# Kernel optimization log

Hardware: AMD Instinct MI355X
Metric: run time of the kernel (lower is better)

## Reference

```python
import jax, jax.numpy as jnp
import numpy as np
import math

BATCH, L, H, P = 8, 2048, 1024, 512
DT_MIN, DT_MAX = 1e-3, 1e-1
STEP_RESCALE = 1.0


def setup_inputs() -> dict:
    key = jax.random.key(0)
    ks = jax.random.split(key, 8)
    signal = jax.random.normal(ks[0], (BATCH, L, H), dtype=jnp.float32)
    prev_state = jnp.zeros((BATCH, P), dtype=jnp.float32)
    # S5-style init: Lambda_re < 0, Lambda_im = pi * k
    Lambda_re = -0.5 * jnp.ones((P,), dtype=jnp.float32)
    Lambda_im = math.pi * jnp.arange(P, dtype=jnp.float32)
    # B stored as real (P,H,2) -> complex B_tilde; lecun scale 1/sqrt(H)
    B = jax.random.normal(ks[1], (P, H, 2), dtype=jnp.float32) / math.sqrt(H)
    # C stored as real (H,P,2) -> complex C_tilde; lecun scale 1/sqrt(P)
    C = jax.random.normal(ks[2], (H, P, 2), dtype=jnp.float32) / math.sqrt(P)
    D = jax.random.normal(ks[3], (H,), dtype=jnp.float32)
    u = jax.random.uniform(ks[4], (P, 1), dtype=jnp.float32)
    log_step = u * (math.log(DT_MAX) - math.log(DT_MIN)) + math.log(DT_MIN)
    return {"signal": signal, "prev_state": prev_state,
            "Lambda_re": Lambda_re, "Lambda_im": Lambda_im,
            "B": B, "C": C, "D": D, "log_step": log_step}


def _binop(qi, qj):
    # parallel-scan combine for diagonal linear recurrence x_t = A_t x_{t-1} + b_t
    A_i, b_i = qi
    A_j, b_j = qj
    return (A_j * A_i, b_j + A_j * b_i)


def reference(signal, prev_state, Lambda_re, Lambda_im, B, C, D, log_step):
    Lambda = Lambda_re + 1j * Lambda_im                      # (P,) complex
    B_tilde = B[..., 0] + 1j * B[..., 1]                     # (P,H)
    C_tilde = C[..., 0] + 1j * C[..., 1]                     # (H,P)
    step = STEP_RESCALE * jnp.exp(log_step[:, 0])            # (P,)
    # zero-order hold discretization
    Lambda_bar = jnp.exp(Lambda * step)                      # (P,)
    B_bar = ((Lambda_bar - 1.0) / Lambda)[:, None] * B_tilde # (P,H)
    # Bu elements: (BATCH, L, P) complex
    Bu = jnp.einsum('blh,ph->blp', signal.astype(B_bar.dtype), B_bar)
    # A elements: Lambda_bar tiled over time; first element carries prev_state
    A_first = (Lambda_bar[None, :] * prev_state.astype(Lambda_bar.dtype))[:, None, :]
    A_rest = jnp.broadcast_to(Lambda_bar, (signal.shape[0], signal.shape[1] - 1, Lambda_bar.shape[0]))
    A = jnp.concatenate([A_first, A_rest], axis=1)           # (BATCH, L, P)
    _, xs = jax.lax.associative_scan(_binop, (A, Bu), axis=1)  # xs: (BATCH, L, P)
    # conj_sym=True -> 2 * Re(C_tilde @ x), plus feedthrough D*u
    y = 2.0 * jnp.einsum('blp,hp->blh', xs, C_tilde).real + D * signal
    state = xs[:, -1]                                        # (BATCH, P) complex
    return y, state
```

## Files before the change

kernel.cpp:

```cpp
#include <hip/hip_runtime.h>
#include <math.h>

#define L_SEQ   2048
#define BATCH_N 8
#define H_DIM   1024
#define P_DIM   512
#define M_DIM   (BATCH_N * L_SEQ)
#define N2      1024
#define NC      32
#define T_CHUNK 64

typedef __attribute__((ext_vector_type(8))) __bf16 bf16x8;
typedef __attribute__((ext_vector_type(4))) float f32x4;

__device__ __forceinline__ unsigned f2bf_bits(float f) {
    unsigned u = __builtin_bit_cast(unsigned, f);
    return (u + 0x7fffu + ((u >> 16) & 1u)) >> 16;
}
__device__ __forceinline__ float bf_lo(unsigned v) {
    return __builtin_bit_cast(float, v << 16);
}
__device__ __forceinline__ float bf_hi(unsigned v) {
    return __builtin_bit_cast(float, v & 0xffff0000u);
}
__device__ __forceinline__ float bf2f(unsigned short u) {
    return __builtin_bit_cast(float, (unsigned)u << 16);
}

#define ASYNC_COPY16(gsrc, ldst)                                            \
    __builtin_amdgcn_global_load_lds(                                       \
        (__attribute__((address_space(1))) void*)(gsrc),                    \
        (__attribute__((address_space(3))) void*)(ldst), 16, 0, 0)

__global__ void setup_lam(const float* __restrict__ Lre_in,
                          const float* __restrict__ Lim_in,
                          const float* __restrict__ log_step,
                          float* __restrict__ lam) {
    int p = blockIdx.x * blockDim.x + threadIdx.x;
    if (p >= P_DIM) return;
    float step = expf(log_step[p]);
    float c = Lre_in[p];
    float d = Lim_in[p];
    float mag = expf(c * step);
    float ang = d * step;
    float lr = mag * cosf(ang);
    float li = mag * sinf(ang);
    float a = lr - 1.0f, b = li;
    float inv = 1.0f / (c * c + d * d);
    lam[p]             = lr;
    lam[P_DIM + p]     = li;
    lam[2 * P_DIM + p] = (a * c + b * d) * inv;
    lam[3 * P_DIM + p] = (b * c - a * d) * inv;
}

__global__ void build_W(const float* __restrict__ B,
                        const float* __restrict__ C,
                        const float* __restrict__ lam,
                        unsigned short* __restrict__ W1,
                        unsigned short* __restrict__ W2) {
    int idx = blockIdx.x * blockDim.x + threadIdx.x;
    if (idx < P_DIM * H_DIM) {
        int p = idx >> 10;
        int h = idx & (H_DIM - 1);
        float bre = B[(size_t)idx * 2];
        float bim = B[(size_t)idx * 2 + 1];
        float gre = lam[2 * P_DIM + p];
        float gim = lam[3 * P_DIM + p];
        W1[(size_t)p * H_DIM + h]           = (unsigned short)f2bf_bits(gre * bre - gim * bim);
        W1[(size_t)(P_DIM + p) * H_DIM + h] = (unsigned short)f2bf_bits(gre * bim + gim * bre);
    } else {
        int j = idx - P_DIM * H_DIM;
        int h = j >> 9;
        int p = j & (P_DIM - 1);
        float cre = C[(size_t)j * 2];
        float cim = C[(size_t)j * 2 + 1];
        W2[(size_t)h * N2 + p]         = (unsigned short)f2bf_bits( 2.0f * cre);
        W2[(size_t)h * N2 + P_DIM + p] = (unsigned short)f2bf_bits(-2.0f * cim);
    }
}

__global__ void convert_sig(const float* __restrict__ in,
                            unsigned short* __restrict__ out) {
    size_t i = ((size_t)blockIdx.x * 256 + threadIdx.x) * 4;
    float4 v = *(const float4*)(in + i);
    ushort4 o;
    o.x = (unsigned short)f2bf_bits(v.x);
    o.y = (unsigned short)f2bf_bits(v.y);
    o.z = (unsigned short)f2bf_bits(v.z);
    o.w = (unsigned short)f2bf_bits(v.w);
    *(ushort4*)(out + i) = o;
}

template <int MODE>
__global__ __launch_bounds__(256, 4) void gemm_mfma(
    const unsigned short* __restrict__ A,
    const unsigned short* __restrict__ W,
    void* __restrict__ Out, int K,
    const float* __restrict__ Dvec, const unsigned short* __restrict__ SigBf)
{
    __shared__ unsigned short smem[128 * 64 * 2];
    unsigned short* As = smem;
    unsigned short* Ws = smem + 128 * 64;

    const int tid  = threadIdx.x;
    const int lane = tid & 63;
    const int wid  = tid >> 6;
    const int wm   = wid >> 1;
    const int wn   = wid & 1;

    const int id  = blockIdx.x;
    const int xcd = id & 7;
    const int j   = id >> 3;
    const int mb  = xcd * 16 + (j >> 3);
    const int nb  = j & 7;
    const int m0 = mb * 128;
    const int n0 = nb * 128;

    const int srow = tid >> 3;
    const int qg   = ((tid & 7) - ((tid >> 4) & 7)) & 7;
    const unsigned short* Abase = A + (size_t)(m0 + srow) * K + qg * 8;
    const unsigned short* Wbase = W + (size_t)(n0 + srow) * K + qg * 8;

    const int fr = lane & 15;
    const int fq = (lane >> 4) & 3;
    const int sw = fr >> 1;

    f32x4 acc[4][4] = {};

    for (int k0 = 0; k0 < K; k0 += 64) {
        __syncthreads();
        #pragma unroll
        for (int i = 0; i < 4; ++i)
            ASYNC_COPY16(Abase + (size_t)(i * 32) * K + k0,
                         As + (size_t)(i * 256 + wid * 64) * 8);
        #pragma unroll
        for (int i = 0; i < 4; ++i)
            ASYNC_COPY16(Wbase + (size_t)(i * 32) * K + k0,
                         Ws + (size_t)(i * 256 + wid * 64) * 8);
        __syncthreads();

        #pragma unroll
        for (int kk = 0; kk < 2; ++kk) {
            bf16x8 af[4], wf[4];
            #pragma unroll
            for (int mi = 0; mi < 4; ++mi) {
                int row = wm * 64 + mi * 16 + fr;
                int sl  = (kk * 4 + fq + sw) & 7;
                af[mi] = *(const bf16x8*)&As[(size_t)row * 64 + sl * 8];
            }
            #pragma unroll
            for (int ni = 0; ni < 4; ++ni) {
                int row = wn * 64 + ni * 16 + fr;
                int sl  = (kk * 4 + fq + sw) & 7;
                wf[ni] = *(const bf16x8*)&Ws[(size_t)row * 64 + sl * 8];
            }
            #pragma unroll
            for (int mi = 0; mi < 4; ++mi)
                #pragma unroll
                for (int ni = 0; ni < 4; ++ni)
                    acc[mi][ni] = __builtin_amdgcn_mfma_f32_16x16x32_bf16(
                        af[mi], wf[ni], acc[mi][ni], 0, 0, 0);
        }
    }

    if (MODE == 0) {
        unsigned short* T = smem;
        #pragma unroll
        for (int h = 0; h < 2; ++h) {
            __syncthreads();
            if (wm == h) {
                #pragma unroll
                for (int mi = 0; mi < 4; ++mi)
                    #pragma unroll
                    for (int ni = 0; ni < 4; ++ni)
                        #pragma unroll
                        for (int r = 0; r < 4; ++r) {
                            int lrow = mi * 16 + fq * 4 + r;
                            int lcol = wn * 64 + ni * 16 + fr;
                            T[lrow * 128 + lcol] =
                                (unsigned short)f2bf_bits(acc[mi][ni][r]);
                        }
            }
            __syncthreads();
            #pragma unroll
            for (int jj = 0; jj < 4; ++jj) {
                int chunk = jj * 256 + tid;
                int row = chunk >> 4;
                int co  = (chunk & 15) * 8;
                *(ulonglong2*)((unsigned short*)Out +
                    (size_t)(m0 + h * 64 + row) * 1024 + n0 + co) =
                    *(const ulonglong2*)&T[row * 128 + co];
            }
        }
    } else {
        float Dl[4];
        #pragma unroll
        for (int ni = 0; ni < 4; ++ni)
            Dl[ni] = Dvec[n0 + wn * 64 + ni * 16 + fr];
        #pragma unroll
        for (int mi = 0; mi < 4; ++mi) {
            #pragma unroll
            for (int ni = 0; ni < 4; ++ni) {
                #pragma unroll
                for (int r = 0; r < 4; ++r) {
                    int row = m0 + wm * 64 + mi * 16 + fq * 4 + r;
                    int col = n0 + wn * 64 + ni * 16 + fr;
                    float v = acc[mi][ni][r];
                    v = fmaf(Dl[ni], bf2f(SigBf[(size_t)row * 1024 + col]), v);
                    ((float*)Out)[(size_t)row * 1024 + col] = v;
                }
            }
        }
    }
}

__global__ __launch_bounds__(256) void scan_sums(
    const unsigned short* __restrict__ Bu, const float* __restrict__ lam,
    float* __restrict__ S)
{
    int b = blockIdx.x, c = blockIdx.y, t = threadIdx.x;
    int p0 = 2 * t, p1 = 2 * t + 1;
    float lr0 = lam[p0], li0 = lam[P_DIM + p0];
    float lr1 = lam[p1], li1 = lam[P_DIM + p1];
    const unsigned* base =
        (const unsigned*)(Bu + ((size_t)b * L_SEQ + (size_t)c * T_CHUNK) * N2);
    float xr0 = 0, xi0 = 0, xr1 = 0, xi1 = 0;
    for (int j0 = 0; j0 < T_CHUNK; j0 += 8) {
        unsigned R[8], I[8];
        #pragma unroll
        for (int j = 0; j < 8; ++j) {
            R[j] = base[(size_t)(j0 + j) * 512 + t];
            I[j] = base[(size_t)(j0 + j) * 512 + 256 + t];
        }
        #pragma unroll
        for (int j = 0; j < 8; ++j) {
            float nr0 = fmaf(lr0, xr0, fmaf(-li0, xi0, bf_lo(R[j])));
            float ni0 = fmaf(lr0, xi0, fmaf( li0, xr0, bf_lo(I[j])));
            float nr1 = fmaf(lr1, xr1, fmaf(-li1, xi1, bf_hi(R[j])));
            float ni1 = fmaf(lr1, xi1, fmaf( li1, xr1, bf_hi(I[j])));
            xr0 = nr0; xi0 = ni0; xr1 = nr1; xi1 = ni1;
        }
    }
    float* Sb = S + ((size_t)(b * NC + c) * 2) * P_DIM;
    Sb[p0] = xr0; Sb[p1] = xr1;
    Sb[P_DIM + p0] = xi0; Sb[P_DIM + p1] = xi1;
}

__global__ __launch_bounds__(512) void scan_carry(
    const float* __restrict__ S, const float* __restrict__ lam,
    float* __restrict__ CIN)
{
    int b = blockIdx.x, p = threadIdx.x;
    float lr = lam[p], li = lam[P_DIM + p];
    float pr = lr, pi = li;
    #pragma unroll
    for (int i = 0; i < 6; ++i) {
        float nr = pr * pr - pi * pi;
        float ni = 2.0f * pr * pi;
        pr = nr; pi = ni;
    }
    float cr = 0, ci = 0;
    for (int c = 0; c < NC; ++c) {
        float* Cb = CIN + ((size_t)(b * NC + c) * 2) * P_DIM;
        Cb[p] = cr; Cb[P_DIM + p] = ci;
        const float* Sb = S + ((size_t)(b * NC + c) * 2) * P_DIM;
        float sr = Sb[p], si = Sb[P_DIM + p];
        float nr = fmaf(pr, cr, fmaf(-pi, ci, sr));
        float ni = fmaf(pr, ci, fmaf( pi, cr, si));
        cr = nr; ci = ni;
    }
}

__global__ __launch_bounds__(256) void scan_apply(
    unsigned short* __restrict__ Bu, const float* __restrict__ lam,
    const float* __restrict__ CIN, float* __restrict__ out_state,
    int interleaved)
{
    int b = blockIdx.x, c = blockIdx.y, t = threadIdx.x;
    int p0 = 2 * t, p1 = 2 * t + 1;
    float lr0 = lam[p0], li0 = lam[P_DIM + p0];
    float lr1 = lam[p1], li1 = lam[P_DIM + p1];
    const float* Cb = CIN + ((size_t)(b * NC + c) * 2) * P_DIM;
    float xr0 = Cb[p0], xi0 = Cb[P_DIM + p0];
    float xr1 = Cb[p1], xi1 = Cb[P_DIM + p1];
    unsigned* base =
        (unsigned*)(Bu + ((size_t)b * L_SEQ + (size_t)c * T_CHUNK) * N2);
    for (int j0 = 0; j0 < T_CHUNK; j0 += 8) {
        unsigned R[8], I[8];
        #pragma unroll
        for (int j = 0; j < 8; ++j) {
            R[j] = base[(size_t)(j0 + j) * 512 + t];
            I[j] = base[(size_t)(j0 + j) * 512 + 256 + t];
        }
        #pragma unroll
        for (int j = 0; j < 8; ++j) {
            float nr0 = fmaf(lr0, xr0, fmaf(-li0, xi0, bf_lo(R[j])));
            float ni0 = fmaf(lr0, xi0, fmaf( li0, xr0, bf_lo(I[j])));
            float nr1 = fmaf(lr1, xr1, fmaf(-li1, xi1, bf_hi(R[j])));
            float ni1 = fmaf(lr1, xi1, fmaf( li1, xr1, bf_hi(I[j])));
            xr0 = nr0; xi0 = ni0; xr1 = nr1; xi1 = ni1;
            R[j] = f2bf_bits(nr0) | (f2bf_bits(nr1) << 16);
            I[j] = f2bf_bits(ni0) | (f2bf_bits(ni1) << 16);
        }
        #pragma unroll
        for (int j = 0; j < 8; ++j) {
            base[(size_t)(j0 + j) * 512 + t]       = R[j];
            base[(size_t)(j0 + j) * 512 + 256 + t] = I[j];
        }
    }
    if (c == NC - 1) {
        if (interleaved) {
            out_state[((size_t)b * P_DIM + p0) * 2]     = xr0;
            out_state[((size_t)b * P_DIM + p0) * 2 + 1] = xi0;
            out_state[((size_t)b * P_DIM + p1) * 2]     = xr1;
            out_state[((size_t)b * P_DIM + p1) * 2 + 1] = xi1;
        } else {
            out_state[(size_t)b * P_DIM + p0] = xr0;
            out_state[(size_t)b * P_DIM + p1] = xr1;
        }
    }
}

extern "C" void kernel_launch(void* const* d_in, const int* in_sizes, int n_in,
                              void* d_out, int out_size, void* d_ws, size_t ws_size,
                              hipStream_t stream)
{
    const float* signal   = (const float*)d_in[0];
    const float* Lre      = (const float*)d_in[2];
    const float* Lim      = (const float*)d_in[3];
    const float* B        = (const float*)d_in[4];
    const float* C        = (const float*)d_in[5];
    const float* Dv       = (const float*)d_in[6];
    const float* log_step = (const float*)d_in[7];

    char* ws = (char*)d_ws;
    unsigned short* sigbf = (unsigned short*)ws;
    unsigned short* Bubf  = (unsigned short*)(ws + 33554432);
    unsigned short* W1bf  = (unsigned short*)(ws + 67108864);
    unsigned short* W2bf  = (unsigned short*)(ws + 69206016);
    float*          lam   = (float*)(ws + 71303168);
    float*          S     = (float*)(ws + 71311360);
    float*          CIN   = (float*)(ws + 71835648);
    size_t need = 72359936;
    if (ws_size < need) return;

    float* y_out = (float*)d_out;
    float* state_out = y_out + (size_t)M_DIM * H_DIM;
    int interleaved = (out_size - M_DIM * H_DIM) >= 2 * BATCH_N * P_DIM;

    setup_lam<<<dim3(2), dim3(256), 0, stream>>>(Lre, Lim, log_step, lam);
    build_W<<<dim3((2 * P_DIM * H_DIM) / 256), dim3(256), 0, stream>>>(
        B, C, lam, W1bf, W2bf);
    convert_sig<<<dim3((M_DIM * H_DIM) / 1024), dim3(256), 0, stream>>>(signal, sigbf);

    gemm_mfma<0><<<dim3(1024), dim3(256), 0, stream>>>(
        sigbf, W1bf, Bubf, H_DIM, nullptr, nullptr);

    scan_sums<<<dim3(BATCH_N, NC), dim3(256), 0, stream>>>(Bubf, lam, S);
    scan_carry<<<dim3(BATCH_N), dim3(512), 0, stream>>>(S, lam, CIN);
    scan_apply<<<dim3(BATCH_N, NC), dim3(256), 0, stream>>>(
        Bubf, lam, CIN, state_out, interleaved);

    gemm_mfma<1><<<dim3(1024), dim3(256), 0, stream>>>(
        Bubf, W2bf, y_out, N2, Dv, sigbf);
}
```

Before: 236.4 us.

## Rewrite GEMM as 256x256 tile, 8-wave, double-buffered ping-pong pipeline

The bf16 MFMA GEMM moves from 128x128 tiles with 4 waves and a single LDS buffer to 256x256 tiles with 8 waves and a double-buffered 128KB LDS stage. Global-to-LDS async copies for the next k-tiles are interleaved between four MFMA quadrants, with explicit barriers, waitcnts and setprio raising wave priority during MFMA bursts. The aim is to hide load latency and raise data reuse per tile. The risks are that the grid shrinks to 256 blocks, which is about one per CU, and that register and LDS pressure grow.

```diff
diff --git a/kernel.cpp b/kernel.cpp
--- a/kernel.cpp
+++ b/kernel.cpp
@@ -92,75 +92,152 @@
 }
 
 template <int MODE>
-__global__ __launch_bounds__(256, 4) void gemm_mfma(
+__global__ __launch_bounds__(512, 2) void gemm_mfma(
     const unsigned short* __restrict__ A,
     const unsigned short* __restrict__ W,
     void* __restrict__ Out, int K,
     const float* __restrict__ Dvec, const unsigned short* __restrict__ SigBf)
 {
-    __shared__ unsigned short smem[128 * 64 * 2];
-    unsigned short* As = smem;
-    unsigned short* Ws = smem + 128 * 64;
+    __shared__ unsigned short smem[65536];
 
     const int tid  = threadIdx.x;
     const int lane = tid & 63;
     const int wid  = tid >> 6;
-    const int wm   = wid >> 1;
-    const int wn   = wid & 1;
+    const int wm   = wid >> 2;
+    const int wn   = wid & 3;
 
     const int id  = blockIdx.x;
-    const int xcd = id & 7;
-    const int j   = id >> 3;
-    const int mb  = xcd * 16 + (j >> 3);
-    const int nb  = j & 7;
-    const int m0 = mb * 128;
-    const int n0 = nb * 128;
-
-    const int srow = tid >> 3;
-    const int qg   = ((tid & 7) - ((tid >> 4) & 7)) & 7;
-    const unsigned short* Abase = A + (size_t)(m0 + srow) * K + qg * 8;
-    const unsigned short* Wbase = W + (size_t)(n0 + srow) * K + qg * 8;
-
-    const int fr = lane & 15;
-    const int fq = (lane >> 4) & 3;
-    const int sw = fr >> 1;
-
-    f32x4 acc[4][4] = {};
-
-    for (int k0 = 0; k0 < K; k0 += 64) {
-        __syncthreads();
-        #pragma unroll
-        for (int i = 0; i < 4; ++i)
-            ASYNC_COPY16(Abase + (size_t)(i * 32) * K + k0,
-                         As + (size_t)(i * 256 + wid * 64) * 8);
-        #pragma unroll
-        for (int i = 0; i < 4; ++i)
-            ASYNC_COPY16(Wbase + (size_t)(i * 32) * K + k0,
-                         Ws + (size_t)(i * 256 + wid * 64) * 8);
-        __syncthreads();
-
-        #pragma unroll
-        for (int kk = 0; kk < 2; ++kk) {
-            bf16x8 af[4], wf[4];
-            #pragma unroll
-            for (int mi = 0; mi < 4; ++mi) {
-                int row = wm * 64 + mi * 16 + fr;
-                int sl  = (kk * 4 + fq + sw) & 7;
-                af[mi] = *(const bf16x8*)&As[(size_t)row * 64 + sl * 8];
-            }
-            #pragma unroll
-            for (int ni = 0; ni < 4; ++ni) {
-                int row = wn * 64 + ni * 16 + fr;
-                int sl  = (kk * 4 + fq + sw) & 7;
-                wf[ni] = *(const bf16x8*)&Ws[(size_t)row * 64 + sl * 8];
-            }
-            #pragma unroll
-            for (int mi = 0; mi < 4; ++mi)
-                #pragma unroll
-                for (int ni = 0; ni < 4; ++ni)
-                    acc[mi][ni] = __builtin_amdgcn_mfma_f32_16x16x32_bf16(
-                        af[mi], wf[ni], acc[mi][ni], 0, 0, 0);
-        }
+    const int wg  = (id & 7) * 32 + (id >> 3);
+    const int m0  = (wg >> 2) * 256;
+    const int n0  = (wg & 3) * 256;
+
+    const int fr  = lane & 15;
+    const int fq  = lane >> 4;
+    const int ks0 = ((fq + (fr >> 1)) & 7) * 8;
+    const int ks1 = ks0 ^ 32;
+    const int qg  = ((tid & 7) - ((tid >> 4) & 7)) & 7;
+
+    const int NKT = K >> 6;
+
+    auto STAGE = [&](const unsigned short* __restrict__ Mat, int mn0,
+                     int half, int kt, int bofs) {
+        const unsigned short* s = Mat
+            + (size_t)(mn0 + half * 128 + (tid >> 3)) * K + (kt << 6) + qg * 8;
+        unsigned short* d = smem + (kt & 1) * 32768 + bofs
+            + (half * 1024 + wid * 64) * 8;
+        ASYNC_COPY16(s, d);
+        ASYNC_COPY16(s + (size_t)64 * K, d + 4096);
+    };
+
+    f32x4 acc[8][4] = {};
+
+    STAGE(A, m0, 0, 0, 0);      STAGE(A, m0, 1, 0, 0);
+    STAGE(W, n0, 0, 0, 16384);  STAGE(W, n0, 1, 0, 16384);
+    STAGE(W, n0, 0, 1, 16384);  STAGE(A, m0, 0, 1, 0);
+    asm volatile("s_waitcnt vmcnt(4)" ::: "memory");
+    __builtin_amdgcn_s_barrier();
+
+    #pragma unroll 1
+    for (int kt = 0; kt < NKT; ++kt) {
+        const unsigned short* Ab =
+            smem + (kt & 1) * 32768 + (wm * 128 + fr) * 64;
+        const unsigned short* Wb =
+            smem + (kt & 1) * 32768 + 16384 + (wn * 64 + fr) * 64;
+        bf16x8 af[4][2], w0[2][2], w1[2][2];
+
+        #pragma unroll
+        for (int mi = 0; mi < 4; ++mi) {
+            af[mi][0] = *(const bf16x8*)&Ab[mi * 1024 + ks0];
+            af[mi][1] = *(const bf16x8*)&Ab[mi * 1024 + ks1];
+        }
+        #pragma unroll
+        for (int ni = 0; ni < 2; ++ni) {
+            w0[ni][0] = *(const bf16x8*)&Wb[ni * 1024 + ks0];
+            w0[ni][1] = *(const bf16x8*)&Wb[ni * 1024 + ks1];
+        }
+        if (kt + 1 < NKT) {
+            STAGE(A, m0, 1, kt + 1, 0);
+            STAGE(W, n0, 1, kt + 1, 16384);
+        }
+        __builtin_amdgcn_s_barrier();
+        asm volatile("s_waitcnt lgkmcnt(0)" ::: "memory");
+        __builtin_amdgcn_sched_barrier(0);
+        __builtin_amdgcn_s_setprio(1);
+        #pragma unroll
+        for (int mi = 0; mi < 4; ++mi)
+            #pragma unroll
+            for (int ni = 0; ni < 2; ++ni) {
+                acc[mi][ni] = __builtin_amdgcn_mfma_f32_16x16x32_bf16(
+                    af[mi][0], w0[ni][0], acc[mi][ni], 0, 0, 0);
+                acc[mi][ni] = __builtin_amdgcn_mfma_f32_16x16x32_bf16(
+                    af[mi][1], w0[ni][1], acc[mi][ni], 0, 0, 0);
+            }
+        __builtin_amdgcn_s_setprio(0);
+        __builtin_amdgcn_s_barrier();
+
+        #pragma unroll
+        for (int ni = 0; ni < 2; ++ni) {
+            w1[ni][0] = *(const bf16x8*)&Wb[(2 + ni) * 1024 + ks0];
+            w1[ni][1] = *(const bf16x8*)&Wb[(2 + ni) * 1024 + ks1];
+        }
+        __builtin_amdgcn_s_barrier();
+        asm volatile("s_waitcnt lgkmcnt(0)" ::: "memory");
+        __builtin_amdgcn_sched_barrier(0);
+        __builtin_amdgcn_s_setprio(1);
+        #pragma unroll
+        for (int mi = 0; mi < 4; ++mi)
+            #pragma unroll
+            for (int ni = 0; ni < 2; ++ni) {
+                acc[mi][2 + ni] = __builtin_amdgcn_mfma_f32_16x16x32_bf16(
+                    af[mi][0], w1[ni][0], acc[mi][2 + ni], 0, 0, 0);
+                acc[mi][2 + ni] = __builtin_amdgcn_mfma_f32_16x16x32_bf16(
+                    af[mi][1], w1[ni][1], acc[mi][2 + ni], 0, 0, 0);
+            }
+        __builtin_amdgcn_s_setprio(0);
+        __builtin_amdgcn_s_barrier();
+
+        #pragma unroll
+        for (int mi = 0; mi < 4; ++mi) {
+            af[mi][0] = *(const bf16x8*)&Ab[4096 + mi * 1024 + ks0];
+            af[mi][1] = *(const bf16x8*)&Ab[4096 + mi * 1024 + ks1];
+        }
+        if (kt + 2 < NKT)
+            STAGE(W, n0, 0, kt + 2, 16384);
+        __builtin_amdgcn_s_barrier();
+        asm volatile("s_waitcnt lgkmcnt(0)" ::: "memory");
+        __builtin_amdgcn_sched_barrier(0);
+        __builtin_amdgcn_s_setprio(1);
+        #pragma unroll
+        for (int mi = 0; mi < 4; ++mi)
+            #pragma unroll
+            for (int ni = 0; ni < 2; ++ni) {
+                acc[4 + mi][ni] = __builtin_amdgcn_mfma_f32_16x16x32_bf16(
+                    af[mi][0], w0[ni][0], acc[4 + mi][ni], 0, 0, 0);
+                acc[4 + mi][ni] = __builtin_amdgcn_mfma_f32_16x16x32_bf16(
+                    af[mi][1], w0[ni][1], acc[4 + mi][ni], 0, 0, 0);
+            }
+        __builtin_amdgcn_s_setprio(0);
+        __builtin_amdgcn_s_barrier();
+
+        if (kt + 2 < NKT)
+            STAGE(A, m0, 0, kt + 2, 0);
+        __builtin_amdgcn_s_barrier();
+        __builtin_amdgcn_s_setprio(1);
+        #pragma unroll
+        for (int mi = 0; mi < 4; ++mi)
+            #pragma unroll
+            for (int ni = 0; ni < 2; ++ni) {
+                acc[4 + mi][2 + ni] = __builtin_amdgcn_mfma_f32_16x16x32_bf16(
+                    af[mi][0], w1[ni][0], acc[4 + mi][2 + ni], 0, 0, 0);
+                acc[4 + mi][2 + ni] = __builtin_amdgcn_mfma_f32_16x16x32_bf16(
+                    af[mi][1], w1[ni][1], acc[4 + mi][2 + ni], 0, 0, 0);
+            }
+        __builtin_amdgcn_s_setprio(0);
+        if (kt == NKT - 2)
+            asm volatile("s_waitcnt vmcnt(0)" ::: "memory");
+        else
+            asm volatile("s_waitcnt vmcnt(4)" ::: "memory");
+        __builtin_amdgcn_s_barrier();
     }
 
     if (MODE == 0) {
@@ -170,26 +247,26 @@
             __syncthreads();
             if (wm == h) {
                 #pragma unroll
-                for (int mi = 0; mi < 4; ++mi)
+                for (int mi = 0; mi < 8; ++mi)
                     #pragma unroll
                     for (int ni = 0; ni < 4; ++ni)
                         #pragma unroll
                         for (int r = 0; r < 4; ++r) {
                             int lrow = mi * 16 + fq * 4 + r;
                             int lcol = wn * 64 + ni * 16 + fr;
-                            T[lrow * 128 + lcol] =
+                            T[lrow * 264 + lcol] =
                                 (unsigned short)f2bf_bits(acc[mi][ni][r]);
                         }
             }
             __syncthreads();
             #pragma unroll
-            for (int jj = 0; jj < 4; ++jj) {
-                int chunk = jj * 256 + tid;
-                int row = chunk >> 4;
-                int co  = (chunk & 15) * 8;
+            for (int jj = 0; jj < 8; ++jj) {
+                int chunk = jj * 512 + tid;
+                int row = chunk >> 5;
+                int co  = (chunk & 31) * 8;
                 *(ulonglong2*)((unsigned short*)Out +
-                    (size_t)(m0 + h * 64 + row) * 1024 + n0 + co) =
-                    *(const ulonglong2*)&T[row * 128 + co];
+                    (size_t)(m0 + h * 128 + row) * 1024 + n0 + co) =
+                    *(const ulonglong2*)&T[row * 264 + co];
             }
         }
     } else {
@@ -198,12 +275,12 @@
         for (int ni = 0; ni < 4; ++ni)
             Dl[ni] = Dvec[n0 + wn * 64 + ni * 16 + fr];
         #pragma unroll
-        for (int mi = 0; mi < 4; ++mi) {
+        for (int mi = 0; mi < 8; ++mi) {
             #pragma unroll
             for (int ni = 0; ni < 4; ++ni) {
                 #pragma unroll
                 for (int r = 0; r < 4; ++r) {
-                    int row = m0 + wm * 64 + mi * 16 + fq * 4 + r;
+                    int row = m0 + wm * 128 + mi * 16 + fq * 4 + r;
                     int col = n0 + wn * 64 + ni * 16 + fr;
                     float v = acc[mi][ni][r];
                     v = fmaf(Dl[ni], bf2f(SigBf[(size_t)row * 1024 + col]), v);
@@ -353,7 +430,7 @@
         B, C, lam, W1bf, W2bf);
     convert_sig<<<dim3((M_DIM * H_DIM) / 1024), dim3(256), 0, stream>>>(signal, sigbf);
 
-    gemm_mfma<0><<<dim3(1024), dim3(256), 0, stream>>>(
+    gemm_mfma<0><<<dim3(256), dim3(512), 0, stream>>>(
         sigbf, W1bf, Bubf, H_DIM, nullptr, nullptr);
 
     scan_sums<<<dim3(BATCH_N, NC), dim3(256), 0, stream>>>(Bubf, lam, S);
@@ -361,6 +438,6 @@
     scan_apply<<<dim3(BATCH_N, NC), dim3(256), 0, stream>>>(
         Bubf, lam, CIN, state_out, interleaved);
 
-    gemm_mfma<1><<<dim3(1024), dim3(256), 0, stream>>>(
+    gemm_mfma<1><<<dim3(256), dim3(512), 0, stream>>>(
         Bubf, W2bf, y_out, N2, Dv, sigbf);
 }
```

Result: slower. 241.9 us (+2.3%).

## Fuse fp32-to-bf16 signal conversion into first GEMM and software-pipeline scan loads

Applied to the files above, without the earlier changes.

Removes the separate convert_sig pass. The first GEMM now reads fp32 signal directly, converts it to bf16 in registers and stores it to LDS. The second GEMM reads the fp32 signal for the D feedthrough term. The scan kernels double-buffer global loads across 8-step groups, and scan_carry preloads all chunk sums into registers. This saves a full 64MB read plus a 32MB write of the signal, but the first GEMM loses its async global-to-LDS copies for A and reads twice as many bytes through registers.

```diff
diff --git a/kernel.cpp b/kernel.cpp
--- a/kernel.cpp
+++ b/kernel.cpp
@@ -22,9 +22,6 @@
 }
 __device__ __forceinline__ float bf_hi(unsigned v) {
     return __builtin_bit_cast(float, v & 0xffff0000u);
-}
-__device__ __forceinline__ float bf2f(unsigned short u) {
-    return __builtin_bit_cast(float, (unsigned)u << 16);
 }
 
 #define ASYNC_COPY16(gsrc, ldst)                                            \
@@ -79,24 +76,12 @@
     }
 }
 
-__global__ void convert_sig(const float* __restrict__ in,
-                            unsigned short* __restrict__ out) {
-    size_t i = ((size_t)blockIdx.x * 256 + threadIdx.x) * 4;
-    float4 v = *(const float4*)(in + i);
-    ushort4 o;
-    o.x = (unsigned short)f2bf_bits(v.x);
-    o.y = (unsigned short)f2bf_bits(v.y);
-    o.z = (unsigned short)f2bf_bits(v.z);
-    o.w = (unsigned short)f2bf_bits(v.w);
-    *(ushort4*)(out + i) = o;
-}
-
 template <int MODE>
 __global__ __launch_bounds__(256, 4) void gemm_mfma(
-    const unsigned short* __restrict__ A,
+    const void* __restrict__ Asrc,
     const unsigned short* __restrict__ W,
     void* __restrict__ Out, int K,
-    const float* __restrict__ Dvec, const unsigned short* __restrict__ SigBf)
+    const float* __restrict__ Dvec, const float* __restrict__ SigF)
 {
     __shared__ unsigned short smem[128 * 64 * 2];
     unsigned short* As = smem;
@@ -118,7 +103,10 @@
 
     const int srow = tid >> 3;
     const int qg   = ((tid & 7) - ((tid >> 4) & 7)) & 7;
-    const unsigned short* Abase = A + (size_t)(m0 + srow) * K + qg * 8;
+    const unsigned short* Abf = (const unsigned short*)Asrc
+        + (size_t)(m0 + srow) * K + qg * 8;
+    const float* Af = (const float*)Asrc
+        + (size_t)(m0 + srow) * K + qg * 8;
     const unsigned short* Wbase = W + (size_t)(n0 + srow) * K + qg * 8;
 
     const int fr = lane & 15;
@@ -131,12 +119,27 @@
         __syncthreads();
         #pragma unroll
         for (int i = 0; i < 4; ++i)
-            ASYNC_COPY16(Abase + (size_t)(i * 32) * K + k0,
-                         As + (size_t)(i * 256 + wid * 64) * 8);
-        #pragma unroll
-        for (int i = 0; i < 4; ++i)
             ASYNC_COPY16(Wbase + (size_t)(i * 32) * K + k0,
                          Ws + (size_t)(i * 256 + wid * 64) * 8);
+        if (MODE == 0) {
+            #pragma unroll
+            for (int i = 0; i < 4; ++i) {
+                const float* s = Af + (size_t)(i * 32) * K + k0;
+                float4 v0 = *(const float4*)s;
+                float4 v1 = *(const float4*)(s + 4);
+                uint4 pk;
+                pk.x = f2bf_bits(v0.x) | (f2bf_bits(v0.y) << 16);
+                pk.y = f2bf_bits(v0.z) | (f2bf_bits(v0.w) << 16);
+                pk.z = f2bf_bits(v1.x) | (f2bf_bits(v1.y) << 16);
+                pk.w = f2bf_bits(v1.z) | (f2bf_bits(v1.w) << 16);
+                *(uint4*)(As + ((size_t)i * 256 + tid) * 8) = pk;
+            }
+        } else {
+            #pragma unroll
+            for (int i = 0; i < 4; ++i)
+                ASYNC_COPY16(Abf + (size_t)(i * 32) * K + k0,
+                             As + (size_t)(i * 256 + wid * 64) * 8);
+        }
         __syncthreads();
 
         #pragma unroll
@@ -206,13 +209,30 @@
                     int row = m0 + wm * 64 + mi * 16 + fq * 4 + r;
                     int col = n0 + wn * 64 + ni * 16 + fr;
                     float v = acc[mi][ni][r];
-                    v = fmaf(Dl[ni], bf2f(SigBf[(size_t)row * 1024 + col]), v);
+                    v = fmaf(Dl[ni], SigF[(size_t)row * 1024 + col], v);
                     ((float*)Out)[(size_t)row * 1024 + col] = v;
                 }
             }
         }
     }
 }
+
+#define SCAN_LOADG(R, I, j0)                                                \
+    _Pragma("unroll")                                                       \
+    for (int j = 0; j < 8; ++j) {                                           \
+        R[j] = base[(size_t)((j0) + j) * 512 + t];                          \
+        I[j] = base[(size_t)((j0) + j) * 512 + 256 + t];                    \
+    }
+
+#define SCAN_COMP(R, I)                                                     \
+    _Pragma("unroll")                                                       \
+    for (int j = 0; j < 8; ++j) {                                           \
+        float nr0 = fmaf(lr0, xr0, fmaf(-li0, xi0, bf_lo(R[j])));           \
+        float ni0 = fmaf(lr0, xi0, fmaf( li0, xr0, bf_lo(I[j])));           \
+        float nr1 = fmaf(lr1, xr1, fmaf(-li1, xi1, bf_hi(R[j])));           \
+        float ni1 = fmaf(lr1, xi1, fmaf( li1, xr1, bf_hi(I[j])));           \
+        xr0 = nr0; xi0 = ni0; xr1 = nr1; xi1 = ni1;                         \
+    }
 
 __global__ __launch_bounds__(256) void scan_sums(
     const unsigned short* __restrict__ Bu, const float* __restrict__ lam,
@@ -225,21 +245,14 @@
     const unsigned* base =
         (const unsigned*)(Bu + ((size_t)b * L_SEQ + (size_t)c * T_CHUNK) * N2);
     float xr0 = 0, xi0 = 0, xr1 = 0, xi1 = 0;
-    for (int j0 = 0; j0 < T_CHUNK; j0 += 8) {
-        unsigned R[8], I[8];
-        #pragma unroll
-        for (int j = 0; j < 8; ++j) {
-            R[j] = base[(size_t)(j0 + j) * 512 + t];
-            I[j] = base[(size_t)(j0 + j) * 512 + 256 + t];
-        }
-        #pragma unroll
-        for (int j = 0; j < 8; ++j) {
-            float nr0 = fmaf(lr0, xr0, fmaf(-li0, xi0, bf_lo(R[j])));
-            float ni0 = fmaf(lr0, xi0, fmaf( li0, xr0, bf_lo(I[j])));
-            float nr1 = fmaf(lr1, xr1, fmaf(-li1, xi1, bf_hi(R[j])));
-            float ni1 = fmaf(lr1, xi1, fmaf( li1, xr1, bf_hi(I[j])));
-            xr0 = nr0; xi0 = ni0; xr1 = nr1; xi1 = ni1;
-        }
+    unsigned R0[8], I0[8], R1[8], I1[8];
+    SCAN_LOADG(R0, I0, 0)
+    #pragma unroll
+    for (int gg = 0; gg < 4; ++gg) {
+        SCAN_LOADG(R1, I1, gg * 16 + 8)
+        SCAN_COMP(R0, I0)
+        if (gg < 3) { SCAN_LOADG(R0, I0, gg * 16 + 16) }
+        SCAN_COMP(R1, I1)
     }
     float* Sb = S + ((size_t)(b * NC + c) * 2) * P_DIM;
     Sb[p0] = xr0; Sb[p1] = xr1;
@@ -259,17 +272,40 @@
         float ni = 2.0f * pr * pi;
         pr = nr; pi = ni;
     }
+    float sr[NC], si[NC];
+    #pragma unroll
+    for (int c = 0; c < NC; ++c) {
+        const float* Sb = S + ((size_t)(b * NC + c) * 2) * P_DIM;
+        sr[c] = Sb[p];
+        si[c] = Sb[P_DIM + p];
+    }
     float cr = 0, ci = 0;
+    #pragma unroll
     for (int c = 0; c < NC; ++c) {
         float* Cb = CIN + ((size_t)(b * NC + c) * 2) * P_DIM;
         Cb[p] = cr; Cb[P_DIM + p] = ci;
-        const float* Sb = S + ((size_t)(b * NC + c) * 2) * P_DIM;
-        float sr = Sb[p], si = Sb[P_DIM + p];
-        float nr = fmaf(pr, cr, fmaf(-pi, ci, sr));
-        float ni = fmaf(pr, ci, fmaf( pi, cr, si));
+        float nr = fmaf(pr, cr, fmaf(-pi, ci, sr[c]));
+        float ni = fmaf(pr, ci, fmaf( pi, cr, si[c]));
         cr = nr; ci = ni;
     }
 }
+
+#define SCAN_COMPST(R, I, j0)                                               \
+    _Pragma("unroll")                                                       \
+    for (int j = 0; j < 8; ++j) {                                           \
+        float nr0 = fmaf(lr0, xr0, fmaf(-li0, xi0, bf_lo(R[j])));           \
+        float ni0 = fmaf(lr0, xi0, fmaf( li0, xr0, bf_lo(I[j])));           \
+        float nr1 = fmaf(lr1, xr1, fmaf(-li1, xi1, bf_hi(R[j])));           \
+        float ni1 = fmaf(lr1, xi1, fmaf( li1, xr1, bf_hi(I[j])));           \
+        xr0 = nr0; xi0 = ni0; xr1 = nr1; xi1 = ni1;                         \
+        R[j] = f2bf_bits(nr0) | (f2bf_bits(nr1) << 16);                     \
+        I[j] = f2bf_bits(ni0) | (f2bf_bits(ni1) << 16);                     \
+    }                                                                       \
+    _Pragma("unroll")                                                       \
+    for (int j = 0; j < 8; ++j) {                                           \
+        base[(size_t)((j0) + j) * 512 + t]       = R[j];                    \
+        base[(size_t)((j0) + j) * 512 + 256 + t] = I[j];                    \
+    }
 
 __global__ __launch_bounds__(256) void scan_apply(
     unsigned short* __restrict__ Bu, const float* __restrict__ lam,
@@ -285,28 +321,14 @@
     float xr1 = Cb[p1], xi1 = Cb[P_DIM + p1];
     unsigned* base =
         (unsigned*)(Bu + ((size_t)b * L_SEQ + (size_t)c * T_CHUNK) * N2);
-    for (int j0 = 0; j0 < T_CHUNK; j0 += 8) {
-        unsigned R[8], I[8];
-        #pragma unroll
-        for (int j = 0; j < 8; ++j) {
-            R[j] = base[(size_t)(j0 + j) * 512 + t];
-            I[j] = base[(size_t)(j0 + j) * 512 + 256 + t];
-        }
-        #pragma unroll
-        for (int j = 0; j < 8; ++j) {
-            float nr0 = fmaf(lr0, xr0, fmaf(-li0, xi0, bf_lo(R[j])));
-            float ni0 = fmaf(lr0, xi0, fmaf( li0, xr0, bf_lo(I[j])));
-            float nr1 = fmaf(lr1, xr1, fmaf(-li1, xi1, bf_hi(R[j])));
-            float ni1 = fmaf(lr1, xi1, fmaf( li1, xr1, bf_hi(I[j])));
-            xr0 = nr0; xi0 = ni0; xr1 = nr1; xi1 = ni1;
-            R[j] = f2bf_bits(nr0) | (f2bf_bits(nr1) << 16);
-            I[j] = f2bf_bits(ni0) | (f2bf_bits(ni1) << 16);
-        }
-        #pragma unroll
-        for (int j = 0; j < 8; ++j) {
-            base[(size_t)(j0 + j) * 512 + t]       = R[j];
-            base[(size_t)(j0 + j) * 512 + 256 + t] = I[j];
-        }
+    unsigned R0[8], I0[8], R1[8], I1[8];
+    SCAN_LOADG(R0, I0, 0)
+    #pragma unroll
+    for (int gg = 0; gg < 4; ++gg) {
+        SCAN_LOADG(R1, I1, gg * 16 + 8)
+        SCAN_COMPST(R0, I0, gg * 16)
+        if (gg < 3) { SCAN_LOADG(R0, I0, gg * 16 + 16) }
+        SCAN_COMPST(R1, I1, gg * 16 + 8)
     }
     if (c == NC - 1) {
         if (interleaved) {
@@ -334,14 +356,13 @@
     const float* log_step = (const float*)d_in[7];
 
     char* ws = (char*)d_ws;
-    unsigned short* sigbf = (unsigned short*)ws;
-    unsigned short* Bubf  = (unsigned short*)(ws + 33554432);
-    unsigned short* W1bf  = (unsigned short*)(ws + 67108864);
-    unsigned short* W2bf  = (unsigned short*)(ws + 69206016);
-    float*          lam   = (float*)(ws + 71303168);
-    float*          S     = (float*)(ws + 71311360);
-    float*          CIN   = (float*)(ws + 71835648);
-    size_t need = 72359936;
+    unsigned short* Bubf  = (unsigned short*)ws;
+    unsigned short* W1bf  = (unsigned short*)(ws + 33554432);
+    unsigned short* W2bf  = (unsigned short*)(ws + 35651584);
+    float*          lam   = (float*)(ws + 37748736);
+    float*          S     = (float*)(ws + 37756928);
+    float*          CIN   = (float*)(ws + 38281216);
+    size_t need = 38805504;
     if (ws_size < need) return;
 
     float* y_out = (float*)d_out;
@@ -351,10 +372,9 @@
     setup_lam<<<dim3(2), dim3(256), 0, stream>>>(Lre, Lim, log_step, lam);
     build_W<<<dim3((2 * P_DIM * H_DIM) / 256), dim3(256), 0, stream>>>(
         B, C, lam, W1bf, W2bf);
-    convert_sig<<<dim3((M_DIM * H_DIM) / 1024), dim3(256), 0, stream>>>(signal, sigbf);
 
     gemm_mfma<0><<<dim3(1024), dim3(256), 0, stream>>>(
-        sigbf, W1bf, Bubf, H_DIM, nullptr, nullptr);
+        signal, W1bf, Bubf, H_DIM, nullptr, nullptr);
 
     scan_sums<<<dim3(BATCH_N, NC), dim3(256), 0, stream>>>(Bubf, lam, S);
     scan_carry<<<dim3(BATCH_N), dim3(512), 0, stream>>>(S, lam, CIN);
@@ -362,5 +382,5 @@
         Bubf, lam, CIN, state_out, interleaved);
 
     gemm_mfma<1><<<dim3(1024), dim3(256), 0, stream>>>(
-        Bubf, W2bf, y_out, N2, Dv, sigbf);
-}
+        Bubf, W2bf, y_out, N2, Dv, signal);
+}
```

New measurement: 250.0 us. 1.06x slower.
